# Performance work log

Measured on AMD Instinct MI355X. Metric: run time of the kernel, lower is better.

## Reference

```python
import jax, jax.numpy as jnp
import numpy as np

D_MODEL = 2048
N_HEADS = 16
D_K = D_MODEL // N_HEADS
MAX_SEQ = 2048
THETA = 10000.0


def _rope(x, token_positions):
    # x: [B, H, S, d_k], token_positions: [S] int
    freqs = 1.0 / THETA ** (jnp.arange(0, D_K, 2, dtype=jnp.float32) / D_K)  # [d_k/2]
    angles = token_positions.astype(jnp.float32)[:, None] * freqs[None, :]   # [S, d_k/2]
    cos, sin = jnp.cos(angles), jnp.sin(angles)
    x_even, x_odd = x[..., 0::2], x[..., 1::2]
    out_even = x_even * cos - x_odd * sin
    out_odd = x_even * sin + x_odd * cos
    return jnp.stack([out_even, out_odd], axis=-1).reshape(x.shape)


def setup_inputs() -> dict:
    key = jax.random.key(0)
    ks = jax.random.split(key, 5)
    B, S = 2, 2048
    std = np.sqrt(2.0 / (D_MODEL + D_MODEL))
    def w(k):
        return (jax.random.truncated_normal(k, -3.0, 3.0, (D_MODEL, D_MODEL), jnp.float32) * std)
    return {
        "x": jax.random.normal(ks[0], (B, S, D_MODEL), jnp.float32),
        "wq": w(ks[1]), "wk": w(ks[2]), "wv": w(ks[3]), "wo": w(ks[4]),
        "token_positions": jnp.arange(S, dtype=jnp.int32),
    }


def reference(x, wq, wk, wv, wo, token_positions):
    B, S, _ = x.shape
    # Linear: einsum('... i, o i -> ... o')
    def proj(w):
        h = jnp.einsum('bsi,oi->bso', x, w)
        return h.reshape(B, S, N_HEADS, D_K).transpose(0, 2, 1, 3)  # [B,H,S,d_k]
    Q, K, V = proj(wq), proj(wk), proj(wv)
    Q = _rope(Q, token_positions)
    K = _rope(K, token_positions)
    scores = jnp.einsum('bhqd,bhkd->bhqk', Q, K) / jnp.sqrt(jnp.float32(D_K))
    causal = jnp.tril(jnp.ones((S, S), dtype=bool))
    scores = jnp.where(causal, scores, -jnp.inf)
    attn = jax.nn.softmax(scores, axis=-1)
    out = jnp.einsum('bhqk,bhkd->bhqd', attn, V)
    out = out.transpose(0, 2, 1, 3).reshape(B, S, D_MODEL)
    return jnp.einsum('bsi,oi->bso', out, wo)
```

## Files before the change

### kernel.cpp

```cpp
#include <hip/hip_runtime.h>
#include <stdint.h>
#include <stddef.h>

typedef unsigned short u16;
typedef unsigned int u32;
typedef __attribute__((ext_vector_type(8))) short s8v;
typedef __attribute__((ext_vector_type(4))) short s4v;
typedef __attribute__((ext_vector_type(4))) float f4v;

#define D_MODEL 2048
#define NH 16
#define DK 128

__device__ __forceinline__ float b2f(u16 u) {
    union { u32 i; float f; } v; v.i = ((u32)u) << 16; return v.f;
}
__device__ __forceinline__ u16 f2b(float f) {
    u32 u = __builtin_bit_cast(u32, f);
    u32 r = (u + 0x7fffu + ((u >> 16) & 1u)) >> 16;
    return (u16)r;
}
__device__ __forceinline__ float fexp2(float x) {
    return __builtin_amdgcn_exp2f(x);
}
__device__ __forceinline__ f4v mfma16(s8v a, s8v b, f4v c) {
    return __builtin_amdgcn_mfma_f32_16x16x32_bf16(a, b, c, 0, 0, 0);
}
__device__ __forceinline__ void gload_lds16(const void* g, void* l) {
    __builtin_amdgcn_global_load_lds(
        (const __attribute__((address_space(1))) u32*)(uintptr_t)g,
        (__attribute__((address_space(3))) u32*)(uintptr_t)l, 16, 0, 0);
}

__device__ __forceinline__ void store_out(u16* p, float v)   { *p = f2b(v); }
__device__ __forceinline__ void store_out(float* p, float v) { *p = v; }

#define SBAR()   asm volatile("s_barrier" ::: "memory")
#define VMCNT(n) asm volatile("s_waitcnt vmcnt(" #n ")" ::: "memory")

__global__ __launch_bounds__(256) void cvt_bf16(
    const float* __restrict__ s0, const float* __restrict__ s1,
    const float* __restrict__ s2, const float* __restrict__ s3,
    const float* __restrict__ s4,
    u16* __restrict__ d0, u16* __restrict__ d1, u16* __restrict__ d2,
    u16* __restrict__ d3, u16* __restrict__ d4,
    int n0, int nw)
{
    const int seg = blockIdx.y;
    const float* s = (seg == 0) ? s0 : (seg == 1) ? s1 : (seg == 2) ? s2 : (seg == 3) ? s3 : s4;
    u16*         d = (seg == 0) ? d0 : (seg == 1) ? d1 : (seg == 2) ? d2 : (seg == 3) ? d3 : d4;
    const int    n = (seg == 0) ? n0 : nw;
    int i = (blockIdx.x * 256 + threadIdx.x) * 8;
    if (i >= n) return;
    f4v a = *(const f4v*)(s + i);
    f4v b = *(const f4v*)(s + i + 4);
    s8v o;
    o[0] = (short)f2b(a[0]); o[1] = (short)f2b(a[1]);
    o[2] = (short)f2b(a[2]); o[3] = (short)f2b(a[3]);
    o[4] = (short)f2b(b[0]); o[5] = (short)f2b(b[1]);
    o[6] = (short)f2b(b[2]); o[7] = (short)f2b(b[3]);
    *(s8v*)(d + i) = o;
}

__global__ __launch_bounds__(256) void rope_table(
    float2* __restrict__ tab, const int* __restrict__ pos, int S)
{
    int idx = blockIdx.x * 256 + threadIdx.x;
    if (idx >= S * 64) return;
    int s  = idx >> 6;
    int ip = idx & 63;
    float freq = __expf((float)ip * -0.14391156831212787f);
    float ang  = (float)pos[s] * freq;
    tab[idx] = make_float2(cosf(ang), sinf(ang));
}

__global__ __launch_bounds__(512) void gemm256(
    const u16* __restrict__ A,
    const u16* __restrict__ B0, const u16* __restrict__ B1,
    u16* __restrict__ C0, u16* __restrict__ C1,
    const float2* __restrict__ rtab, int Sdim,
    int M, int N, int K)
{
    const int z = blockIdx.z;
    const u16* Bp = (z == 0) ? B0 : B1;
    u16*       Cp = (z == 0) ? C0 : C1;

    __shared__ short As[2 * 256 * 64];
    __shared__ short Bs[2 * 256 * 64];

    const int t    = threadIdx.x;
    const int lane = t & 63;
    const int w    = t >> 6;
    const int wr   = w >> 2;
    const int wc   = w & 3;
    const int m0   = blockIdx.x * 256;
    const int n0   = blockIdx.y * 256;

    const int srow = t >> 3;
    const int scol = (((t & 7) ^ ((t >> 3) & 7)) * 8);

    const u16* gA = A  + (size_t)(m0 + srow) * K + scol;
    const u16* gB = Bp + (size_t)(n0 + srow) * K + scol;
    char* lA = (char*)As + (size_t)w * 1024;
    char* lB = (char*)Bs + (size_t)w * 1024;
    const size_t rstep = (size_t)64 * K;

    const int fr = lane & 15;
    const int g4 = lane >> 4;
    const int xa = fr & 7;

    f4v acc[8][4];
#pragma unroll
    for (int i = 0; i < 8; i++)
#pragma unroll
        for (int j = 0; j < 4; j++) acc[i][j] = (f4v){0.f, 0.f, 0.f, 0.f};

    auto stageA = [&](int p, int kt, int h) {
        const u16* g = gA + (size_t)kt * 64;
#pragma unroll
        for (int j = 0; j < 2; j++)
            gload_lds16(g + (size_t)(2 * h + j) * rstep,
                        lA + p * 32768 + (2 * h + j) * 8192);
    };
    auto stageB = [&](int p, int kt, int h) {
        const u16* g = gB + (size_t)kt * 64;
#pragma unroll
        for (int j = 0; j < 2; j++)
            gload_lds16(g + (size_t)(2 * h + j) * rstep,
                        lB + p * 32768 + (2 * h + j) * 8192);
    };
    auto loadA = [&](int p, int mh, int ks, s8v* aF) {
        const short* base = As + p * 16384;
        const int sl = ((ks * 4 + g4) ^ xa) * 8;
#pragma unroll
        for (int mi = 0; mi < 4; mi++)
            aF[mi] = *(const s8v*)&base[(wr * 128 + mh * 64 + mi * 16 + fr) * 64 + sl];
    };
    auto loadB = [&](int p, int ks, s8v* bF) {
        const short* base = Bs + p * 16384;
        const int sl = ((ks * 4 + g4) ^ xa) * 8;
#pragma unroll
        for (int ni = 0; ni < 4; ni++)
            bF[ni] = *(const s8v*)&base[(wc * 64 + ni * 16 + fr) * 64 + sl];
    };
    auto mfc = [&](int mh, s8v* aF, s8v* bF) {
        __builtin_amdgcn_s_setprio(1);
#pragma unroll
        for (int mi = 0; mi < 4; mi++)
#pragma unroll
            for (int ni = 0; ni < 4; ni++)
                acc[mh * 4 + mi][ni] = mfma16(aF[mi], bF[ni], acc[mh * 4 + mi][ni]);
        __builtin_amdgcn_s_setprio(0);
    };

    const int NT = K / 64;
    const int NI = NT / 2;

    stageB(0, 0, 0); stageB(0, 0, 1); stageA(0, 0, 0); stageA(0, 0, 1);
    stageB(1, 1, 0);
    VMCNT(2);
    SBAR();

    for (int i = 0; i < NI; i++) {
        const int k1 = 2 * i + 1;
        const int k2 = (2 * i + 2 < NT) ? 2 * i + 2 : 0;
        const int k3 = (2 * i + 3 < NT) ? 2 * i + 3 : 1;
        s8v aF[4], bF[4];

        loadA(0, 0, 0, aF); loadB(0, 0, bF);
        stageB(1, k1, 1);
        VMCNT(4); SBAR();
        mfc(0, aF, bF);
        SBAR();
        loadA(0, 1, 0, aF);
        stageA(1, k1, 0);
        SBAR();
        mfc(1, aF, bF);
        SBAR();
        loadA(0, 0, 1, aF); loadB(0, 1, bF);
        stageA(1, k1, 1);
        SBAR();
        mfc(0, aF, bF);
        SBAR();
        loadA(0, 1, 1, aF);
        stageB(0, k2, 0);
        VMCNT(2); SBAR();
        mfc(1, aF, bF);
        SBAR();
        loadA(1, 0, 0, aF); loadB(1, 0, bF);
        stageB(0, k2, 1);
        VMCNT(4); SBAR();
        mfc(0, aF, bF);
        SBAR();
        loadA(1, 1, 0, aF);
        stageA(0, k2, 0);
        SBAR();
        mfc(1, aF, bF);
        SBAR();
        loadA(1, 0, 1, aF); loadB(1, 1, bF);
        stageA(0, k2, 1);
        SBAR();
        mfc(0, aF, bF);
        SBAR();
        loadA(1, 1, 1, aF);
        stageB(1, k3, 0);
        VMCNT(2); SBAR();
        mfc(1, aF, bF);
        SBAR();
    }
    VMCNT(0);

    const int rg = g4 * 4;
    const float scale = (z == 0) ? 0.12751919968793342f : 1.0f;
    const int srow_b = (m0 % Sdim) + wr * 128;
#pragma unroll
    for (int mit = 0; mit < 8; mit++)
#pragma unroll
        for (int ni = 0; ni < 4; ni++) {
            const int col = n0 + wc * 64 + ni * 16 + fr;
            const int ip  = (col & 127) >> 1;
            const int odd = col & 1;
            size_t base = (size_t)(m0 + wr * 128 + mit * 16 + rg) * N + col;
            const int sr = srow_b + mit * 16 + rg;
#pragma unroll
            for (int r = 0; r < 4; r++) {
                float2 cs = rtab[(size_t)(sr + r) * 64 + ip];
                float v  = acc[mit][ni][r];
                float pv = __shfl_xor(v, 1);
                float o  = odd ? (pv * cs.y + v * cs.x)
                               : (v * cs.x - pv * cs.y);
                Cp[base + (size_t)r * N] = f2b(o * scale);
            }
        }
}

template<typename OutT, int MODE>
__global__ __launch_bounds__(512) void gemm128(
    const u16* __restrict__ A, const u16* __restrict__ Bp,
    OutT* __restrict__ Cp, int M, int N, int K, int Sdim)
{
    __shared__ short As[3 * 256 * 64];
    __shared__ short Bs[3 * 128 * 64];

    const int t    = threadIdx.x;
    const int lane = t & 63;
    const int w    = t >> 6;
    const int wr   = w >> 1;
    const int wc   = w & 1;
    const int m0   = blockIdx.x * 256;
    const int n0   = blockIdx.y * 128;

    const int srow = t >> 3;
    const int scol = (((t & 7) ^ ((t >> 3) & 7)) * 8);

    const u16* gA = A  + (size_t)(m0 + srow) * K + scol;
    const u16* gB = Bp + (size_t)(n0 + srow) * K + scol;
    char* lA = (char*)As + (size_t)w * 1024;
    char* lB = (char*)Bs + (size_t)w * 1024;
    const size_t rstep = (size_t)64 * K;

    const int fr = lane & 15;
    const int g4 = lane >> 4;
    const int xa = fr & 7;

    f4v acc[4][4];
#pragma unroll
    for (int i = 0; i < 4; i++)
#pragma unroll
        for (int j = 0; j < 4; j++) acc[i][j] = (f4v){0.f, 0.f, 0.f, 0.f};

    auto stageA = [&](int p, int kt, int h) {
        const u16* g = gA + (size_t)kt * 64;
#pragma unroll
        for (int j = 0; j < 2; j++)
            gload_lds16(g + (size_t)(2 * h + j) * rstep,
                        lA + p * 32768 + (2 * h + j) * 8192);
    };
    auto stageB = [&](int p, int kt) {
        const u16* g = gB + (size_t)kt * 64;
#pragma unroll
        for (int j = 0; j < 2; j++)
            gload_lds16(g + (size_t)j * rstep,
                        lB + p * 16384 + j * 8192);
    };
    auto loadA = [&](int p, int mh, int ks, s8v* aF) {
        const short* base = As + p * 16384;
        const int sl = ((ks * 4 + g4) ^ xa) * 8;
#pragma unroll
        for (int j = 0; j < 2; j++)
            aF[j] = *(const s8v*)&base[(wr * 64 + (mh * 2 + j) * 16 + fr) * 64 + sl];
    };
    auto loadB = [&](int p, int ks, s8v* bF) {
        const short* base = Bs + p * 8192;
        const int sl = ((ks * 4 + g4) ^ xa) * 8;
#pragma unroll
        for (int ni = 0; ni < 4; ni++)
            bF[ni] = *(const s8v*)&base[(wc * 64 + ni * 16 + fr) * 64 + sl];
    };
    auto mfc = [&](int mh, s8v* aF, s8v* bF) {
        __builtin_amdgcn_s_setprio(1);
#pragma unroll
        for (int j = 0; j < 2; j++)
#pragma unroll
            for (int ni = 0; ni < 4; ni++)
                acc[mh * 2 + j][ni] = mfma16(aF[j], bF[ni], acc[mh * 2 + j][ni]);
        __builtin_amdgcn_s_setprio(0);
    };

    const int NT = K / 64;
    const int NI = NT / 2;

    stageA(0, 0, 0); stageA(0, 0, 1); stageB(0, 0);
    stageA(1, 1, 0); stageA(1, 1, 1); stageB(1, 1);
    VMCNT(6);
    SBAR();

    int s0 = 0, s1 = 1, s2 = 2;
    for (int i = 0; i < NI; i++) {
        const int k2 = (2 * i + 2 < NT) ? 2 * i + 2 : 0;
        const int k3 = (2 * i + 3 < NT) ? 2 * i + 3 : 1;
        s8v aF[2], bF[4];

        loadB(s0, 0, bF); loadA(s0, 0, 0, aF);
        stageA(s2, k2, 0);
        SBAR(); mfc(0, aF, bF); SBAR();
        loadA(s0, 1, 0, aF);
        stageA(s2, k2, 1);
        SBAR(); mfc(1, aF, bF); SBAR();
        loadB(s0, 1, bF); loadA(s0, 0, 1, aF);
        stageB(s2, k2);
        SBAR(); mfc(0, aF, bF); SBAR();
        loadA(s0, 1, 1, aF);
        VMCNT(6); SBAR(); mfc(1, aF, bF); SBAR();
        loadB(s1, 0, bF); loadA(s1, 0, 0, aF);
        stageA(s0, k3, 0);
        SBAR(); mfc(0, aF, bF); SBAR();
        loadA(s1, 1, 0, aF);
        stageA(s0, k3, 1);
        SBAR(); mfc(1, aF, bF); SBAR();
        loadB(s1, 1, bF); loadA(s1, 0, 1, aF);
        stageB(s0, k3);
        SBAR(); mfc(0, aF, bF); SBAR();
        loadA(s1, 1, 1, aF);
        VMCNT(6); SBAR(); mfc(1, aF, bF); SBAR();

        const int ns0 = s2, ns1 = s0, ns2 = s1;
        s0 = ns0; s1 = ns1; s2 = ns2;
    }
    VMCNT(0);

    const int rg = g4 * 4;
    if constexpr (MODE == 0) {
#pragma unroll
        for (int mi = 0; mi < 4; mi++)
#pragma unroll
            for (int ni = 0; ni < 4; ni++) {
                size_t base = (size_t)(m0 + wr * 64 + mi * 16 + rg) * N
                            + (n0 + wc * 64 + ni * 16 + fr);
#pragma unroll
                for (int r = 0; r < 4; r++)
                    store_out(&Cp[base + (size_t)r * N], acc[mi][ni][r]);
            }
    } else {
        __syncthreads();
        short* OT = As;
        const int OP = 264;
#pragma unroll
        for (int mi = 0; mi < 4; mi++)
#pragma unroll
            for (int ni = 0; ni < 4; ni++) {
                s4v pk;
                pk[0] = (short)f2b(acc[mi][ni][0]);
                pk[1] = (short)f2b(acc[mi][ni][1]);
                pk[2] = (short)f2b(acc[mi][ni][2]);
                pk[3] = (short)f2b(acc[mi][ni][3]);
                *(s4v*)&OT[(wc * 64 + ni * 16 + fr) * OP + (wr * 64 + mi * 16 + rg)] = pk;
            }
        __syncthreads();
        const int bb = m0 / Sdim;
        const int sb = m0 % Sdim;
        u16* Vt = (u16*)Cp;
#pragma unroll
        for (int ps = 0; ps < 8; ps++) {
            int idx  = ps * 512 + t;
            int orow = idx >> 5;
            int sc8  = (idx & 31) * 8;
            s8v v = *(const s8v*)&OT[orow * OP + sc8];
            *(s8v*)(Vt + ((size_t)bb * D_MODEL + n0 + orow) * Sdim + sb + sc8) = v;
        }
    }
}

#define AKV 64
#define VP  72
#define PP  72

__global__ __launch_bounds__(512) void attn_kernel(
    const u16* __restrict__ Qg, const u16* __restrict__ Kg,
    const u16* __restrict__ Vtg, u16* __restrict__ Og, int S)
{
    __shared__ short Kbuf[2][64 * 128];
    __shared__ short Vbuf[2][128 * VP];
    __shared__ short Ps[8][16 * PP];

    const int t    = threadIdx.x;
    const int lane = t & 63;
    const int w    = t >> 6;
    const int fr   = lane & 15;
    const int g4   = lane >> 4;
    const int xfr  = (fr & 7) << 3;

    const int d_ = blockIdx.x;
    const int tt = d_ >> 3;
    const int G  = ((tt & 3) << 3) | (d_ & 7);
    const int p  = tt >> 2;
    const int h  = G & 15;
    const int b  = G >> 4;
    const int ntq = S / 128;

    const u16* Qb  = Qg + ((size_t)b * S) * D_MODEL + (size_t)h * DK;
    const u16* Kb  = Kg + ((size_t)b * S) * D_MODEL + (size_t)h * DK;
    const u16* Vtb = Vtg + ((size_t)b * D_MODEL + (size_t)h * DK) * S;
    u16*       Ob  = Og + ((size_t)b * S) * D_MODEL + (size_t)h * DK;

    const int krow = t >> 4;
    const int kc8  = (t & 15) * 8;
    const int kxor = (krow & 7) << 3;
    const int vd   = t >> 3;
    const int vk8  = (t & 7) * 8;

    const int wq64 = (w >> 2) * 64;

    for (int half = 0; half < 2; half++) {
        const int T   = half ? (ntq - 1 - p) : p;
        const int q0  = T * 128;
        const int nkv = 2 * T + 2;

        s8v qf[4];
#pragma unroll
        for (int ks = 0; ks < 4; ks++)
            qf[ks] = *(const s8v*)(Qb +
                (size_t)(q0 + w * 16 + fr) * D_MODEL + ks * 32 + g4 * 8);

        s8v kreg[2], vreg[2];
#pragma unroll
        for (int c = 0; c < 2; c++) {
            kreg[c] = *(const s8v*)(Kb + (size_t)(krow + 32 * c) * D_MODEL + kc8);
            vreg[c] = *(const s8v*)(Vtb + (size_t)(vd + 64 * c) * S + vk8);
        }
        __syncthreads();
#pragma unroll
        for (int c = 0; c < 2; c++)
            *(s8v*)&Kbuf[0][(krow + 32 * c) * 128 + (kc8 ^ kxor)] = kreg[c];
#pragma unroll
        for (int c = 0; c < 2; c++)
            *(s8v*)&Vbuf[0][(vd + 64 * c) * VP + vk8] = vreg[c];
        __syncthreads();

        float m_st = -1e30f, l_st = 0.f;
        f4v accO[8];
#pragma unroll
        for (int df = 0; df < 8; df++) accO[df] = (f4v){0.f, 0.f, 0.f, 0.f};
        const int qg = q0 + w * 16 + fr;

        for (int kt = 0; kt < nkv; kt++) {
            const int  kv0  = kt * AKV;
            const int  buf  = kt & 1;
            const bool last = (kt + 1 == nkv);
            const bool act  = (kv0 <= q0 + wq64);

            if (!last) {
                const size_t kvn = (size_t)(kt + 1) * AKV;
#pragma unroll
                for (int c = 0; c < 2; c++) {
                    kreg[c] = *(const s8v*)(Kb + (kvn + krow + 32 * c) * D_MODEL + kc8);
                    vreg[c] = *(const s8v*)(Vtb + (size_t)(vd + 64 * c) * S + kvn + vk8);
                }
            }

            if (act) {
                f4v sacc[4];
#pragma unroll
                for (int i = 0; i < 4; i++) sacc[i] = (f4v){0.f, 0.f, 0.f, 0.f};
                __builtin_amdgcn_s_setprio(1);
#pragma unroll
                for (int ks = 0; ks < 4; ks++) {
#pragma unroll
                    for (int kf = 0; kf < 4; kf++) {
                        s8v kfr = *(const s8v*)&Kbuf[buf][(kf * 16 + fr) * 128 +
                                                         ((ks * 32 + g4 * 8) ^ xfr)];
                        sacc[kf] = mfma16(kfr, qf[ks], sacc[kf]);
                    }
                }
                __builtin_amdgcn_s_setprio(0);

                if (kv0 == q0 + wq64) {
#pragma unroll
                    for (int kf = 0; kf < 4; kf++)
#pragma unroll
                        for (int r = 0; r < 4; r++)
                            if (kv0 + kf * 16 + g4 * 4 + r > qg)
                                sacc[kf][r] = -1e30f;
                }
                float rm = -1e30f;
#pragma unroll
                for (int kf = 0; kf < 4; kf++)
                    rm = fmaxf(rm, fmaxf(fmaxf(sacc[kf][0], sacc[kf][1]),
                                         fmaxf(sacc[kf][2], sacc[kf][3])));
                rm = fmaxf(rm, __shfl_xor(rm, 16));
                rm = fmaxf(rm, __shfl_xor(rm, 32));
                if (__any(rm > m_st)) {
                    float mn   = fmaxf(m_st, rm);
                    float corr = fexp2(m_st - mn);
                    l_st *= corr;
#pragma unroll
                    for (int df = 0; df < 8; df++) {
                        accO[df][0] *= corr; accO[df][1] *= corr;
                        accO[df][2] *= corr; accO[df][3] *= corr;
                    }
                    m_st = mn;
                }
                float rsum = 0.f;
#pragma unroll
                for (int kf = 0; kf < 4; kf++) {
                    float p0 = fexp2(sacc[kf][0] - m_st);
                    float p1 = fexp2(sacc[kf][1] - m_st);
                    float p2 = fexp2(sacc[kf][2] - m_st);
                    float p3 = fexp2(sacc[kf][3] - m_st);
                    rsum += (p0 + p1) + (p2 + p3);
                    s4v pk;
                    pk[0] = (short)f2b(p0); pk[1] = (short)f2b(p1);
                    pk[2] = (short)f2b(p2); pk[3] = (short)f2b(p3);
                    *(s4v*)&Ps[w][fr * PP + kf * 16 + g4 * 4] = pk;
                }
                rsum += __shfl_xor(rsum, 16);
                rsum += __shfl_xor(rsum, 32);
                l_st += rsum;

                __builtin_amdgcn_s_setprio(1);
#pragma unroll
                for (int ks = 0; ks < 2; ks++) {
                    s8v pf = *(const s8v*)&Ps[w][fr * PP + ks * 32 + g4 * 8];
#pragma unroll
                    for (int df = 0; df < 8; df++) {
                        s8v vf = *(const s8v*)&Vbuf[buf][(df * 16 + fr) * VP +
                                                         ks * 32 + g4 * 8];
                        accO[df] = mfma16(vf, pf, accO[df]);
                    }
                }
                __builtin_amdgcn_s_setprio(0);
            }

            if (!last) {
#pragma unroll
                for (int c = 0; c < 2; c++)
                    *(s8v*)&Kbuf[buf ^ 1][(krow + 32 * c) * 128 + (kc8 ^ kxor)] = kreg[c];
#pragma unroll
                for (int c = 0; c < 2; c++)
                    *(s8v*)&Vbuf[buf ^ 1][(vd + 64 * c) * VP + vk8] = vreg[c];
            }
            __syncthreads();
        }

        float inv = 1.f / l_st;
        short* OL = (short*)&Kbuf[0][0];
#pragma unroll
        for (int df = 0; df < 8; df++) {
            s4v ov;
            ov[0] = (short)f2b(accO[df][0] * inv);
            ov[1] = (short)f2b(accO[df][1] * inv);
            ov[2] = (short)f2b(accO[df][2] * inv);
            ov[3] = (short)f2b(accO[df][3] * inv);
            *(s4v*)&OL[(w * 16 + fr) * 128 + ((df * 16 + g4 * 4) ^ xfr)] = ov;
        }
        __syncthreads();
#pragma unroll
        for (int i = 0; i < 4; i++) {
            int row = i * 32 + (t >> 4);
            int ch  = (t & 15) * 8;
            s8v v = *(const s8v*)&OL[row * 128 + (ch ^ ((row & 7) << 3))];
            *(s8v*)(Ob + (size_t)(q0 + row) * D_MODEL + ch) = v;
        }
    }
}

extern "C" void kernel_launch(void* const* d_in, const int* in_sizes, int n_in,
                              void* d_out, int out_size, void* d_ws, size_t ws_size,
                              hipStream_t stream)
{
    const float* x  = (const float*)d_in[0];
    const float* wq = (const float*)d_in[1];
    const float* wk = (const float*)d_in[2];
    const float* wv = (const float*)d_in[3];
    const float* wo = (const float*)d_in[4];
    const int*   tp = (const int*)d_in[5];

    const int S  = in_sizes[5];
    const int BS = in_sizes[0] / D_MODEL;
    const int Bn = BS / S;
    const int NW = D_MODEL * D_MODEL;
    const int NX = BS * D_MODEL;

    u16* Qw  = (u16*)d_ws;
    u16* Kw  = Qw + (size_t)NX;
    u16* Vw  = Kw + (size_t)NX;
    u16* Xb  = Vw + (size_t)NX;
    u16* Wqb = Xb + (size_t)NX;
    u16* Wkb = Wqb + (size_t)NW;
    u16* Wvb = Wkb + (size_t)NW;
    u16* Wob = Wvb + (size_t)NW;
    float2* Rt = (float2*)(Wob + (size_t)NW);

    {
        dim3 g((NX / 8 + 255) / 256, 5);
        cvt_bf16<<<g, 256, 0, stream>>>(x, wq, wk, wv, wo,
                                        Xb, Wqb, Wkb, Wvb, Wob, NX, NW);
    }

    rope_table<<<(S * 64 + 255) / 256, 256, 0, stream>>>(Rt, tp, S);

    dim3 gqk(BS / 256, D_MODEL / 256, 2);
    gemm256<<<gqk, 512, 0, stream>>>(Xb, Wqb, Wkb, Qw, Kw, Rt, S,
                                     BS, D_MODEL, D_MODEL);

    dim3 gv(BS / 256, D_MODEL / 128, 1);
    gemm128<u16, 1><<<gv, 512, 0, stream>>>(Xb, Wvb, Vw, BS, D_MODEL, D_MODEL, S);

    attn_kernel<<<dim3((S / 256) * NH * Bn, 1, 1), 512, 0, stream>>>(Qw, Kw, Vw, Xb, S);

    dim3 go(BS / 256, D_MODEL / 128, 1);
    gemm128<float, 0><<<go, 512, 0, stream>>>(Xb, Wob, (float*)d_out,
                                              BS, D_MODEL, D_MODEL, S);
}
```

Measured before the change: 229.8 us.

## Single-buffer attention K/V LDS tiles to allow more resident blocks

Replaces the double-buffered K and V shared-memory tiles with single buffers in one flat LDS array, and adds __launch_bounds__(512,4) to request more resident workgroups per CU. The global prefetch into registers is kept, but each iteration now needs an extra barrier before overwriting the tiles. The aim is to cut LDS use (about 53KB per block) so more waves can hide latency. The cost is one more __syncthreads per KV tile and tighter register limits, which could cause spills.

```diff
diff --git a/kernel.cpp b/kernel.cpp
--- a/kernel.cpp
+++ b/kernel.cpp
@@ -395,13 +395,15 @@
 #define VP  72
 #define PP  72
 
-__global__ __launch_bounds__(512) void attn_kernel(
+__global__ __launch_bounds__(512, 4) void attn_kernel(
     const u16* __restrict__ Qg, const u16* __restrict__ Kg,
     const u16* __restrict__ Vtg, u16* __restrict__ Og, int S)
 {
-    __shared__ short Kbuf[2][64 * 128];
-    __shared__ short Vbuf[2][128 * VP];
-    __shared__ short Ps[8][16 * PP];
+    __shared__ short smem[8192 + 9216 + 9216];
+    short* Kl = smem;
+    short* Vl = smem + 8192;
+    short* Pl = smem + 8192 + 9216;
+    short* OL = smem;
 
     const int t    = threadIdx.x;
     const int lane = t & 63;
@@ -430,6 +432,7 @@
     const int vk8  = (t & 7) * 8;
 
     const int wq64 = (w >> 2) * 64;
+    short* Pw = Pl + w * (16 * PP);
 
     for (int half = 0; half < 2; half++) {
         const int T   = half ? (ntq - 1 - p) : p;
@@ -451,10 +454,10 @@
         __syncthreads();
 #pragma unroll
         for (int c = 0; c < 2; c++)
-            *(s8v*)&Kbuf[0][(krow + 32 * c) * 128 + (kc8 ^ kxor)] = kreg[c];
+            *(s8v*)&Kl[(krow + 32 * c) * 128 + (kc8 ^ kxor)] = kreg[c];
 #pragma unroll
         for (int c = 0; c < 2; c++)
-            *(s8v*)&Vbuf[0][(vd + 64 * c) * VP + vk8] = vreg[c];
+            *(s8v*)&Vl[(vd + 64 * c) * VP + vk8] = vreg[c];
         __syncthreads();
 
         float m_st = -1e30f, l_st = 0.f;
@@ -465,7 +468,6 @@
 
         for (int kt = 0; kt < nkv; kt++) {
             const int  kv0  = kt * AKV;
-            const int  buf  = kt & 1;
             const bool last = (kt + 1 == nkv);
             const bool act  = (kv0 <= q0 + wq64);
 
@@ -487,8 +489,8 @@
                 for (int ks = 0; ks < 4; ks++) {
 #pragma unroll
                     for (int kf = 0; kf < 4; kf++) {
-                        s8v kfr = *(const s8v*)&Kbuf[buf][(kf * 16 + fr) * 128 +
-                                                         ((ks * 32 + g4 * 8) ^ xfr)];
+                        s8v kfr = *(const s8v*)&Kl[(kf * 16 + fr) * 128 +
+                                                   ((ks * 32 + g4 * 8) ^ xfr)];
                         sacc[kf] = mfma16(kfr, qf[ks], sacc[kf]);
                     }
                 }
@@ -531,7 +533,7 @@
                     s4v pk;
                     pk[0] = (short)f2b(p0); pk[1] = (short)f2b(p1);
                     pk[2] = (short)f2b(p2); pk[3] = (short)f2b(p3);
-                    *(s4v*)&Ps[w][fr * PP + kf * 16 + g4 * 4] = pk;
+                    *(s4v*)&Pw[fr * PP + kf * 16 + g4 * 4] = pk;
                 }
                 rsum += __shfl_xor(rsum, 16);
                 rsum += __shfl_xor(rsum, 32);
@@ -540,30 +542,30 @@
                 __builtin_amdgcn_s_setprio(1);
 #pragma unroll
                 for (int ks = 0; ks < 2; ks++) {
-                    s8v pf = *(const s8v*)&Ps[w][fr * PP + ks * 32 + g4 * 8];
+                    s8v pf = *(const s8v*)&Pw[fr * PP + ks * 32 + g4 * 8];
 #pragma unroll
                     for (int df = 0; df < 8; df++) {
-                        s8v vf = *(const s8v*)&Vbuf[buf][(df * 16 + fr) * VP +
-                                                         ks * 32 + g4 * 8];
+                        s8v vf = *(const s8v*)&Vl[(df * 16 + fr) * VP +
+                                                  ks * 32 + g4 * 8];
                         accO[df] = mfma16(vf, pf, accO[df]);
                     }
                 }
                 __builtin_amdgcn_s_setprio(0);
             }
 
+            __syncthreads();
             if (!last) {
 #pragma unroll
                 for (int c = 0; c < 2; c++)
-                    *(s8v*)&Kbuf[buf ^ 1][(krow + 32 * c) * 128 + (kc8 ^ kxor)] = kreg[c];
+                    *(s8v*)&Kl[(krow + 32 * c) * 128 + (kc8 ^ kxor)] = kreg[c];
 #pragma unroll
                 for (int c = 0; c < 2; c++)
-                    *(s8v*)&Vbuf[buf ^ 1][(vd + 64 * c) * VP + vk8] = vreg[c];
+                    *(s8v*)&Vl[(vd + 64 * c) * VP + vk8] = vreg[c];
+                __syncthreads();
             }
-            __syncthreads();
         }
 
         float inv = 1.f / l_st;
-        short* OL = (short*)&Kbuf[0][0];
 #pragma unroll
         for (int df = 0; df < 8; df++) {
             s4v ov;
```

New measurement: 242.7 us. +5.6%, slower.
